# Kernel tuning notes

Hardware: AMD Instinct MI355X
Metric: run time of the kernel (lower is better)

The kernel has to match this reference:

```python
import math
import jax, jax.numpy as jnp
import numpy as np

POS_DIM = 32


def _fourier_features(pos, dim):
    # pos: [B, M] in [0,1] -> [B, M, dim]
    half = dim // 2
    freqs = jnp.exp(jnp.linspace(0.0, math.log(1000.0), half, dtype=pos.dtype))
    ang = pos[..., None] * freqs                      # [B, M, half]
    out = jnp.concatenate([jnp.sin(ang), jnp.cos(ang)], axis=-1)
    if out.shape[-1] < dim:  # pad if dim is odd (not the case for dim=32)
        pad = jnp.zeros(out.shape[:-1] + (dim - out.shape[-1],), dtype=pos.dtype)
        out = jnp.concatenate([out, pad], axis=-1)
    return out


def setup_inputs() -> dict:
    key = jax.random.key(0)
    k1, k2, k3 = jax.random.split(key, 3)
    B, T, D, M = 8, 8192, 512, 512
    frame_emb = jax.random.normal(k1, (B, T, D), dtype=jnp.float32)
    beat_bounds = jax.random.randint(k2, (B, M, 2), 0, T).astype(jnp.int64)
    # nn.Linear(D + POS_DIM, D): store as [in, out] for x @ W + b
    bound = 1.0 / math.sqrt(D + POS_DIM)
    W = jax.random.uniform(k3, (D + POS_DIM, D), dtype=jnp.float32,
                           minval=-bound, maxval=bound)
    b = jnp.zeros((D,), dtype=jnp.float32)
    return {"frame_emb": frame_emb, "beat_bounds": beat_bounds, "W": W, "b": b}


def reference(frame_emb, beat_bounds, W, b):
    B, T, D = frame_emb.shape
    M = beat_bounds.shape[1]
    dt = frame_emb.dtype

    # clamp bounds exactly as the torch loop does
    s = jnp.clip(beat_bounds[..., 0], 0, T - 1)                 # [B, M]
    e = jnp.maximum(s + 1, jnp.minimum(beat_bounds[..., 1], T))  # [B, M]

    # segment mean via exclusive cumsum: sum(frame_emb[b, s:e]) = cs[e] - cs[s]
    cs = jnp.concatenate(
        [jnp.zeros((B, 1, D), dtype=dt), jnp.cumsum(frame_emb, axis=1)], axis=1
    )  # [B, T+1, D]
    seg_sum = (jnp.take_along_axis(cs, e[..., None], axis=1)
               - jnp.take_along_axis(cs, s[..., None], axis=1))   # [B, M, D]
    counts = (e - s).astype(dt)[..., None]
    out = seg_sum / counts

    # fourier position features over beat index
    pos = (jnp.arange(M, dtype=dt) / max(1, M - 1)).clip(0.0, 1.0)  # [M]
    ff = _fourier_features(jnp.broadcast_to(pos[None, :], (B, M)), POS_DIM)
    out = jnp.concatenate([out, ff], axis=-1) @ W + b               # [B, M, D]
    return out
```

## Files before the change

kernel.cpp:

```cpp
#include <hip/hip_runtime.h>
#include <math.h>

#define B 8
#define T 8192
#define D 512
#define M 512
#define POS 32
#define CHUNK 16
#define NCHUNK (T / CHUNK)
#define GRP 16
#define NGRP (NCHUNK / GRP)
#define BM (B * M)
#define KD 512

typedef __attribute__((ext_vector_type(8))) short short8;
typedef __attribute__((ext_vector_type(4))) float floatx4;

static __device__ inline unsigned short f2bf(float f) {
    unsigned int u = __float_as_uint(f);
    unsigned int r = (u + 0x7fffu + ((u >> 16) & 1u)) >> 16;
    return (unsigned short)r;
}
static __device__ inline float bf2f(unsigned short h) {
    return __uint_as_float(((unsigned int)h) << 16);
}

__global__ __launch_bounds__(64) void k_scanchunk(const float* __restrict__ fe,
                                                  float* __restrict__ cp,
                                                  float* __restrict__ gsum) {
    int blk = blockIdx.x;
    int b = blk >> 6;
    int g = (blk >> 1) & 31;
    int h = blk & 1;
    int d4 = (h << 8) + (threadIdx.x << 2);

    const float* src = fe + ((size_t)(b * T + g * (GRP * CHUNK)) * D + d4);
    float* cpb = cp + ((size_t)b * NCHUNK + (size_t)g * GRP) * D + d4;

    float4 acc = {0.f, 0.f, 0.f, 0.f};
#pragma unroll 2
    for (int c = 0; c < GRP; ++c) {
#pragma unroll
        for (int r = 0; r < CHUNK; ++r) {
            float4 v = *(const float4*)(src + (size_t)(c * CHUNK + r) * D);
            acc.x += v.x; acc.y += v.y; acc.z += v.z; acc.w += v.w;
        }
        *(float4*)(cpb + (size_t)c * D) = acc;
    }
    *(float4*)(gsum + ((size_t)b * NGRP + g) * D + d4) = acc;
}

__global__ __launch_bounds__(128) void k_scan_coarse(const float* __restrict__ gsum,
                                                     float* __restrict__ gx) {
    int b = blockIdx.x;
    int d4 = threadIdx.x << 2;
    float4 acc = {0.f, 0.f, 0.f, 0.f};
#pragma unroll
    for (int g = 0; g < NGRP; ++g) {
        *(float4*)(gx + ((size_t)b * (NGRP + 1) + g) * D + d4) = acc;
        float4 v = *(const float4*)(gsum + ((size_t)b * NGRP + g) * D + d4);
        acc.x += v.x; acc.y += v.y; acc.z += v.z; acc.w += v.w;
    }
    *(float4*)(gx + ((size_t)b * (NGRP + 1) + NGRP) * D + d4) = acc;
}

__global__ __launch_bounds__(256) void k_wsplit(const float* __restrict__ W,
                                                short* __restrict__ WhT,
                                                short* __restrict__ WlT) {
    __shared__ float ws[32][65];
    int k0 = (blockIdx.x & 15) * 32;
    int n0 = (blockIdx.x >> 4) * 64;
    int t = threadIdx.x;
    {
        int kk = t >> 3;
        int nn = (t & 7) << 3;
        const float* src = W + (size_t)(k0 + kk) * D + n0 + nn;
        float4 v0 = *(const float4*)src;
        float4 v1 = *(const float4*)(src + 4);
        ws[kk][nn + 0] = v0.x; ws[kk][nn + 1] = v0.y; ws[kk][nn + 2] = v0.z; ws[kk][nn + 3] = v0.w;
        ws[kk][nn + 4] = v1.x; ws[kk][nn + 5] = v1.y; ws[kk][nn + 6] = v1.z; ws[kk][nn + 7] = v1.w;
    }
    __syncthreads();
    int n = t >> 2;
    int kq = (t & 3) << 3;
    short8 hv, lv;
#pragma unroll
    for (int j = 0; j < 8; ++j) {
        float w = ws[kq + j][n];
        unsigned short hb = f2bf(w);
        hv[j] = (short)hb;
        lv[j] = (short)f2bf(w - bf2f(hb));
    }
    size_t off = (size_t)(n0 + n) * KD + k0 + kq;
    *(short8*)(WhT + off) = hv;
    *(short8*)(WlT + off) = lv;
}

__global__ __launch_bounds__(128) void k_ffout(const float* __restrict__ W,
                                               const float* __restrict__ bias,
                                               float* __restrict__ ffout) {
    int m = blockIdx.x;
    int n4 = threadIdx.x << 2;
    float pos = (float)m * (1.0f / 511.0f);
    float4 acc = *(const float4*)(bias + n4);
#pragma unroll
    for (int j = 0; j < 16; ++j) {
        float freq = expf(0.46051701859880914f * (float)j);
        float ang = pos * freq;
        float s = sinf(ang), c = cosf(ang);
        float4 wsn = *(const float4*)(W + (size_t)(D + j) * D + n4);
        float4 wcn = *(const float4*)(W + (size_t)(D + 16 + j) * D + n4);
        acc.x += s * wsn.x + c * wcn.x;
        acc.y += s * wsn.y + c * wcn.y;
        acc.z += s * wsn.z + c * wcn.z;
        acc.w += s * wsn.w + c * wcn.w;
    }
    *(float4*)(ffout + (size_t)m * D + n4) = acc;
}

__global__ __launch_bounds__(128) void k_buildx(const float* __restrict__ fe,
                                                const int* __restrict__ bounds,
                                                const float* __restrict__ cp,
                                                const float* __restrict__ gx,
                                                short* __restrict__ Xh,
                                                short* __restrict__ Xl) {
    int bm = blockIdx.x;
    int b = bm / M;
    int b0 = bounds[bm * 2 + 0];
    int b1 = bounds[bm * 2 + 1];
    int s = min(max(b0, 0), T - 1);
    int e = max(min(b1, T), s + 1);
    int cs_ = s >> 4, ce = e >> 4;
    int d4 = threadIdx.x << 2;

    const float* cpb = cp + (size_t)b * NCHUNK * D;
    const float* gxb = gx + (size_t)b * (NGRP + 1) * D;

    float4 acc = *(const float4*)(gxb + (size_t)(ce >> 4) * D + d4);
    if (ce & 15) {
        float4 v = *(const float4*)(cpb + (size_t)(ce - 1) * D + d4);
        acc.x += v.x; acc.y += v.y; acc.z += v.z; acc.w += v.w;
    }
    {
        float4 p = *(const float4*)(gxb + (size_t)(cs_ >> 4) * D + d4);
        acc.x -= p.x; acc.y -= p.y; acc.z -= p.z; acc.w -= p.w;
        if (cs_ & 15) {
            float4 v = *(const float4*)(cpb + (size_t)(cs_ - 1) * D + d4);
            acc.x -= v.x; acc.y -= v.y; acc.z -= v.z; acc.w -= v.w;
        }
    }

    const float* feb = fe + (size_t)b * T * D + d4;
    for (int t = ce * CHUNK; t < e; ++t) {
        float4 v = *(const float4*)(feb + (size_t)t * D);
        acc.x += v.x; acc.y += v.y; acc.z += v.z; acc.w += v.w;
    }
    for (int t = cs_ * CHUNK; t < s; ++t) {
        float4 v = *(const float4*)(feb + (size_t)t * D);
        acc.x -= v.x; acc.y -= v.y; acc.z -= v.z; acc.w -= v.w;
    }
    float inv = 1.0f / (float)(e - s);
    float x0 = acc.x * inv, x1 = acc.y * inv, x2 = acc.z * inv, x3 = acc.w * inv;

    unsigned short h0 = f2bf(x0), h1 = f2bf(x1), h2 = f2bf(x2), h3 = f2bf(x3);
    typedef __attribute__((ext_vector_type(4))) short short4v;
    short4v hv, lv;
    hv[0] = (short)h0; hv[1] = (short)h1; hv[2] = (short)h2; hv[3] = (short)h3;
    lv[0] = (short)f2bf(x0 - bf2f(h0));
    lv[1] = (short)f2bf(x1 - bf2f(h1));
    lv[2] = (short)f2bf(x2 - bf2f(h2));
    lv[3] = (short)f2bf(x3 - bf2f(h3));
    size_t off = (size_t)bm * KD + d4;
    *(short4v*)(Xh + off) = hv;
    *(short4v*)(Xl + off) = lv;
}

__global__ __launch_bounds__(256) void k_gemm(const short* __restrict__ Xh,
                                              const short* __restrict__ Xl,
                                              const short* __restrict__ WhT,
                                              const short* __restrict__ WlT,
                                              const float* __restrict__ ffout,
                                              float* __restrict__ out) {
    __shared__ short Ah[64 * 32], Al[64 * 32], Bh[64 * 32], Bl[64 * 32];
    int n0 = (blockIdx.x & 7) << 6;
    int m0 = (blockIdx.x >> 3) << 6;
    int tid = threadIdx.x;
    int w = tid >> 6;
    int l = tid & 63;
    int lm = l & 15;
    int q = l >> 4;
    int wm = (w & 1) << 5;
    int wn = (w >> 1) << 5;

    floatx4 acc[2][2];
#pragma unroll
    for (int i = 0; i < 2; ++i)
#pragma unroll
        for (int j = 0; j < 2; ++j)
            acc[i][j] = (floatx4){0.f, 0.f, 0.f, 0.f};

    int srow = tid >> 2;
    int skq = tid & 3;
    int sslot = skq ^ ((srow >> 1) & 3);
    int ldsoff = (srow << 5) + (sslot << 3);
    const short* gXh = Xh + (size_t)(m0 + srow) * KD + (skq << 3);
    const short* gXl = Xl + (size_t)(m0 + srow) * KD + (skq << 3);
    const short* gBh = WhT + (size_t)(n0 + srow) * KD + (skq << 3);
    const short* gBl = WlT + (size_t)(n0 + srow) * KD + (skq << 3);

    int aoff[2], boff[2];
#pragma unroll
    for (int mt = 0; mt < 2; ++mt) {
        int row = wm + (mt << 4) + lm;
        aoff[mt] = (row << 5) + ((q ^ ((row >> 1) & 3)) << 3);
    }
#pragma unroll
    for (int nt = 0; nt < 2; ++nt) {
        int row = wn + (nt << 4) + lm;
        boff[nt] = (row << 5) + ((q ^ ((row >> 1) & 3)) << 3);
    }

    for (int k0 = 0; k0 < KD; k0 += 32) {
        short8 vxh = *(const short8*)(gXh + k0);
        short8 vxl = *(const short8*)(gXl + k0);
        short8 vbh = *(const short8*)(gBh + k0);
        short8 vbl = *(const short8*)(gBl + k0);
        __syncthreads();
        *(short8*)(Ah + ldsoff) = vxh;
        *(short8*)(Al + ldsoff) = vxl;
        *(short8*)(Bh + ldsoff) = vbh;
        *(short8*)(Bl + ldsoff) = vbl;
        __syncthreads();

        short8 ah[2], al[2], bh[2], bl[2];
#pragma unroll
        for (int mt = 0; mt < 2; ++mt) {
            ah[mt] = *(const short8*)(Ah + aoff[mt]);
            al[mt] = *(const short8*)(Al + aoff[mt]);
        }
#pragma unroll
        for (int nt = 0; nt < 2; ++nt) {
            bh[nt] = *(const short8*)(Bh + boff[nt]);
            bl[nt] = *(const short8*)(Bl + boff[nt]);
        }
#pragma unroll
        for (int mt = 0; mt < 2; ++mt)
#pragma unroll
            for (int nt = 0; nt < 2; ++nt) {
                acc[mt][nt] = __builtin_amdgcn_mfma_f32_16x16x32_bf16(
                    ah[mt], bh[nt], acc[mt][nt], 0, 0, 0);
                acc[mt][nt] = __builtin_amdgcn_mfma_f32_16x16x32_bf16(
                    ah[mt], bl[nt], acc[mt][nt], 0, 0, 0);
                acc[mt][nt] = __builtin_amdgcn_mfma_f32_16x16x32_bf16(
                    al[mt], bh[nt], acc[mt][nt], 0, 0, 0);
            }
    }

#pragma unroll
    for (int mt = 0; mt < 2; ++mt) {
#pragma unroll
        for (int nt = 0; nt < 2; ++nt) {
            int gcol = n0 + wn + (nt << 4) + lm;
#pragma unroll
            for (int r = 0; r < 4; ++r) {
                int grow = m0 + wm + (mt << 4) + (q << 2) + r;
                float f = ffout[(size_t)(grow & (M - 1)) * D + gcol];
                out[(size_t)grow * D + gcol] = acc[mt][nt][r] + f;
            }
        }
    }
}

extern "C" void kernel_launch(void* const* d_in, const int* in_sizes, int n_in,
                              void* d_out, int out_size, void* d_ws, size_t ws_size,
                              hipStream_t stream) {
    const float* fe = (const float*)d_in[0];
    const int* bounds = (const int*)d_in[1];
    const float* W = (const float*)d_in[2];
    const float* bias = (const float*)d_in[3];
    float* out = (float*)d_out;

    float* cp = (float*)d_ws;
    float* gsum = cp + (size_t)B * NCHUNK * D;
    float* gx = gsum + (size_t)B * NGRP * D;
    float* ffout = gx + (size_t)B * (NGRP + 1) * D;
    short* Xh = (short*)(ffout + (size_t)M * D);
    short* Xl = Xh + (size_t)BM * KD;
    short* WhT = Xl + (size_t)BM * KD;
    short* WlT = WhT + (size_t)KD * D;

    k_scanchunk<<<B * NGRP * 2, 64, 0, stream>>>(fe, cp, gsum);
    k_scan_coarse<<<B, 128, 0, stream>>>(gsum, gx);
    k_wsplit<<<128, 256, 0, stream>>>(W, WhT, WlT);
    k_ffout<<<M, 128, 0, stream>>>(W, bias, ffout);
    k_buildx<<<BM, 128, 0, stream>>>(fe, bounds, cp, gx, Xh, Xl);
    k_gemm<<<64 * 8, 256, 0, stream>>>(Xh, Xl, WhT, WlT, ffout, out);
}
```

Baseline: 248.1 us.

## Fuse scan, weight split and fourier projection into one launch; shrink scan chunks

Merges the chunk-scan, weight bf16 split and fourier-feature projection kernels into a single launch that branches on block index, removing two launches and letting the independent work run concurrently. Chunk size drops from 16 to 4 and groups grow to 32, so the segment-mean step scans at most 3 leftover raw rows per endpoint instead of 15. The scan now uses 256 threads handling float2 per block over 512 blocks. The cost is a chunk-prefix workspace four times larger, so more scan output is written and read, and the per-thread loads are narrower.

```diff
diff --git a/kernel.cpp b/kernel.cpp
--- a/kernel.cpp
+++ b/kernel.cpp
@@ -6,14 +6,15 @@
 #define D 512
 #define M 512
 #define POS 32
-#define CHUNK 16
+#define CHUNK 4
 #define NCHUNK (T / CHUNK)
-#define GRP 16
+#define GRP 32
 #define NGRP (NCHUNK / GRP)
 #define BM (B * M)
 #define KD 512
 
 typedef __attribute__((ext_vector_type(8))) short short8;
+typedef __attribute__((ext_vector_type(4))) short short4v;
 typedef __attribute__((ext_vector_type(4))) float floatx4;
 
 static __device__ inline unsigned short f2bf(float f) {
@@ -25,97 +26,94 @@
     return __uint_as_float(((unsigned int)h) << 16);
 }
 
-__global__ __launch_bounds__(64) void k_scanchunk(const float* __restrict__ fe,
-                                                  float* __restrict__ cp,
-                                                  float* __restrict__ gsum) {
+__global__ __launch_bounds__(256) void k_fusedA(const float* __restrict__ fe,
+                                                const float* __restrict__ W,
+                                                const float* __restrict__ bias,
+                                                float* __restrict__ cp,
+                                                float* __restrict__ gsum,
+                                                short* __restrict__ WhT,
+                                                short* __restrict__ WlT,
+                                                float* __restrict__ ffout) {
     int blk = blockIdx.x;
-    int b = blk >> 6;
-    int g = (blk >> 1) & 31;
-    int h = blk & 1;
-    int d4 = (h << 8) + (threadIdx.x << 2);
-
-    const float* src = fe + ((size_t)(b * T + g * (GRP * CHUNK)) * D + d4);
-    float* cpb = cp + ((size_t)b * NCHUNK + (size_t)g * GRP) * D + d4;
-
-    float4 acc = {0.f, 0.f, 0.f, 0.f};
-#pragma unroll 2
-    for (int c = 0; c < GRP; ++c) {
-#pragma unroll
-        for (int r = 0; r < CHUNK; ++r) {
-            float4 v = *(const float4*)(src + (size_t)(c * CHUNK + r) * D);
-            acc.x += v.x; acc.y += v.y; acc.z += v.z; acc.w += v.w;
-        }
-        *(float4*)(cpb + (size_t)c * D) = acc;
-    }
-    *(float4*)(gsum + ((size_t)b * NGRP + g) * D + d4) = acc;
-}
-
-__global__ __launch_bounds__(128) void k_scan_coarse(const float* __restrict__ gsum,
+    int tid = threadIdx.x;
+    if (blk < 512) {
+        int b = blk >> 6;
+        int g = blk & 63;
+        int d2 = tid << 1;
+        const float* src = fe + ((size_t)(b * T + g * (GRP * CHUNK)) * D + d2);
+        float* cpb = cp + ((size_t)b * NCHUNK + (size_t)g * GRP) * D + d2;
+        float2 acc = {0.f, 0.f};
+#pragma unroll 4
+        for (int c = 0; c < GRP; ++c) {
+#pragma unroll
+            for (int r = 0; r < CHUNK; ++r) {
+                float2 v = *(const float2*)(src + (size_t)(c * CHUNK + r) * D);
+                acc.x += v.x; acc.y += v.y;
+            }
+            *(float2*)(cpb + (size_t)c * D) = acc;
+        }
+        *(float2*)(gsum + ((size_t)b * NGRP + g) * D + d2) = acc;
+    } else if (blk < 640) {
+        __shared__ float ws[32][65];
+        int wb = blk - 512;
+        int k0 = (wb & 15) * 32;
+        int n0 = (wb >> 4) * 64;
+        {
+            int kk = tid >> 3;
+            int nn = (tid & 7) << 3;
+            const float* src = W + (size_t)(k0 + kk) * D + n0 + nn;
+            float4 v0 = *(const float4*)src;
+            float4 v1 = *(const float4*)(src + 4);
+            ws[kk][nn + 0] = v0.x; ws[kk][nn + 1] = v0.y; ws[kk][nn + 2] = v0.z; ws[kk][nn + 3] = v0.w;
+            ws[kk][nn + 4] = v1.x; ws[kk][nn + 5] = v1.y; ws[kk][nn + 6] = v1.z; ws[kk][nn + 7] = v1.w;
+        }
+        __syncthreads();
+        int n = tid >> 2;
+        int kq = (tid & 3) << 3;
+        short8 hv, lv;
+#pragma unroll
+        for (int j = 0; j < 8; ++j) {
+            float w = ws[kq + j][n];
+            unsigned short hb = f2bf(w);
+            hv[j] = (short)hb;
+            lv[j] = (short)f2bf(w - bf2f(hb));
+        }
+        size_t off = (size_t)(n0 + n) * KD + k0 + kq;
+        *(short8*)(WhT + off) = hv;
+        *(short8*)(WlT + off) = lv;
+    } else {
+        int m = ((blk - 640) << 1) + (tid >> 7);
+        int n4 = (tid & 127) << 2;
+        float pos = (float)m * (1.0f / 511.0f);
+        float4 acc = *(const float4*)(bias + n4);
+#pragma unroll
+        for (int j = 0; j < 16; ++j) {
+            float freq = expf(0.46051701859880914f * (float)j);
+            float ang = pos * freq;
+            float s = sinf(ang), c = cosf(ang);
+            float4 wsn = *(const float4*)(W + (size_t)(D + j) * D + n4);
+            float4 wcn = *(const float4*)(W + (size_t)(D + 16 + j) * D + n4);
+            acc.x += s * wsn.x + c * wcn.x;
+            acc.y += s * wsn.y + c * wcn.y;
+            acc.z += s * wsn.z + c * wcn.z;
+            acc.w += s * wsn.w + c * wcn.w;
+        }
+        *(float4*)(ffout + (size_t)m * D + n4) = acc;
+    }
+}
+
+__global__ __launch_bounds__(256) void k_scan_coarse(const float* __restrict__ gsum,
                                                      float* __restrict__ gx) {
     int b = blockIdx.x;
-    int d4 = threadIdx.x << 2;
-    float4 acc = {0.f, 0.f, 0.f, 0.f};
+    int d2 = threadIdx.x << 1;
+    float2 acc = {0.f, 0.f};
 #pragma unroll
     for (int g = 0; g < NGRP; ++g) {
-        *(float4*)(gx + ((size_t)b * (NGRP + 1) + g) * D + d4) = acc;
-        float4 v = *(const float4*)(gsum + ((size_t)b * NGRP + g) * D + d4);
-        acc.x += v.x; acc.y += v.y; acc.z += v.z; acc.w += v.w;
-    }
-    *(float4*)(gx + ((size_t)b * (NGRP + 1) + NGRP) * D + d4) = acc;
-}
-
-__global__ __launch_bounds__(256) void k_wsplit(const float* __restrict__ W,
-                                                short* __restrict__ WhT,
-                                                short* __restrict__ WlT) {
-    __shared__ float ws[32][65];
-    int k0 = (blockIdx.x & 15) * 32;
-    int n0 = (blockIdx.x >> 4) * 64;
-    int t = threadIdx.x;
-    {
-        int kk = t >> 3;
-        int nn = (t & 7) << 3;
-        const float* src = W + (size_t)(k0 + kk) * D + n0 + nn;
-        float4 v0 = *(const float4*)src;
-        float4 v1 = *(const float4*)(src + 4);
-        ws[kk][nn + 0] = v0.x; ws[kk][nn + 1] = v0.y; ws[kk][nn + 2] = v0.z; ws[kk][nn + 3] = v0.w;
-        ws[kk][nn + 4] = v1.x; ws[kk][nn + 5] = v1.y; ws[kk][nn + 6] = v1.z; ws[kk][nn + 7] = v1.w;
-    }
-    __syncthreads();
-    int n = t >> 2;
-    int kq = (t & 3) << 3;
-    short8 hv, lv;
-#pragma unroll
-    for (int j = 0; j < 8; ++j) {
-        float w = ws[kq + j][n];
-        unsigned short hb = f2bf(w);
-        hv[j] = (short)hb;
-        lv[j] = (short)f2bf(w - bf2f(hb));
-    }
-    size_t off = (size_t)(n0 + n) * KD + k0 + kq;
-    *(short8*)(WhT + off) = hv;
-    *(short8*)(WlT + off) = lv;
-}
-
-__global__ __launch_bounds__(128) void k_ffout(const float* __restrict__ W,
-                                               const float* __restrict__ bias,
-                                               float* __restrict__ ffout) {
-    int m = blockIdx.x;
-    int n4 = threadIdx.x << 2;
-    float pos = (float)m * (1.0f / 511.0f);
-    float4 acc = *(const float4*)(bias + n4);
-#pragma unroll
-    for (int j = 0; j < 16; ++j) {
-        float freq = expf(0.46051701859880914f * (float)j);
-        float ang = pos * freq;
-        float s = sinf(ang), c = cosf(ang);
-        float4 wsn = *(const float4*)(W + (size_t)(D + j) * D + n4);
-        float4 wcn = *(const float4*)(W + (size_t)(D + 16 + j) * D + n4);
-        acc.x += s * wsn.x + c * wcn.x;
-        acc.y += s * wsn.y + c * wcn.y;
-        acc.z += s * wsn.z + c * wcn.z;
-        acc.w += s * wsn.w + c * wcn.w;
-    }
-    *(float4*)(ffout + (size_t)m * D + n4) = acc;
+        *(float2*)(gx + ((size_t)b * (NGRP + 1) + g) * D + d2) = acc;
+        float2 v = *(const float2*)(gsum + ((size_t)b * NGRP + g) * D + d2);
+        acc.x += v.x; acc.y += v.y;
+    }
+    *(float2*)(gx + ((size_t)b * (NGRP + 1) + NGRP) * D + d2) = acc;
 }
 
 __global__ __launch_bounds__(128) void k_buildx(const float* __restrict__ fe,
@@ -130,21 +128,21 @@
     int b1 = bounds[bm * 2 + 1];
     int s = min(max(b0, 0), T - 1);
     int e = max(min(b1, T), s + 1);
-    int cs_ = s >> 4, ce = e >> 4;
+    int cs_ = s >> 2, ce = e >> 2;
     int d4 = threadIdx.x << 2;
 
     const float* cpb = cp + (size_t)b * NCHUNK * D;
     const float* gxb = gx + (size_t)b * (NGRP + 1) * D;
 
-    float4 acc = *(const float4*)(gxb + (size_t)(ce >> 4) * D + d4);
-    if (ce & 15) {
+    float4 acc = *(const float4*)(gxb + (size_t)(ce >> 5) * D + d4);
+    if (ce & 31) {
         float4 v = *(const float4*)(cpb + (size_t)(ce - 1) * D + d4);
         acc.x += v.x; acc.y += v.y; acc.z += v.z; acc.w += v.w;
     }
     {
-        float4 p = *(const float4*)(gxb + (size_t)(cs_ >> 4) * D + d4);
+        float4 p = *(const float4*)(gxb + (size_t)(cs_ >> 5) * D + d4);
         acc.x -= p.x; acc.y -= p.y; acc.z -= p.z; acc.w -= p.w;
-        if (cs_ & 15) {
+        if (cs_ & 31) {
             float4 v = *(const float4*)(cpb + (size_t)(cs_ - 1) * D + d4);
             acc.x -= v.x; acc.y -= v.y; acc.z -= v.z; acc.w -= v.w;
         }
@@ -163,7 +161,6 @@
     float x0 = acc.x * inv, x1 = acc.y * inv, x2 = acc.z * inv, x3 = acc.w * inv;
 
     unsigned short h0 = f2bf(x0), h1 = f2bf(x1), h2 = f2bf(x2), h3 = f2bf(x3);
-    typedef __attribute__((ext_vector_type(4))) short short4v;
     short4v hv, lv;
     hv[0] = (short)h0; hv[1] = (short)h1; hv[2] = (short)h2; hv[3] = (short)h3;
     lv[0] = (short)f2bf(x0 - bf2f(h0));
@@ -289,10 +286,8 @@
     short* WhT = Xl + (size_t)BM * KD;
     short* WlT = WhT + (size_t)KD * D;
 
-    k_scanchunk<<<B * NGRP * 2, 64, 0, stream>>>(fe, cp, gsum);
-    k_scan_coarse<<<B, 128, 0, stream>>>(gsum, gx);
-    k_wsplit<<<128, 256, 0, stream>>>(W, WhT, WlT);
-    k_ffout<<<M, 128, 0, stream>>>(W, bias, ffout);
+    k_fusedA<<<896, 256, 0, stream>>>(fe, W, bias, cp, gsum, WhT, WlT, ffout);
+    k_scan_coarse<<<B, 256, 0, stream>>>(gsum, gx);
     k_buildx<<<BM, 128, 0, stream>>>(fe, bounds, cp, gx, Xh, Xl);
     k_gemm<<<64 * 8, 256, 0, stream>>>(Xh, Xl, WhT, WlT, ffout, out);
 }
```

Result: faster. 230.7 us (-7.0%).
